# Kernel optimization log

Measured on AMD Instinct MI355X. Metric: run time of the kernel, lower is better.

The kernel has to match this reference:

```python
import jax, jax.numpy as jnp
import numpy as np

D_MODEL, D_STATE, D_CONV, EXPAND = 1024, 16, 4, 2
D_INNER = D_MODEL * EXPAND
BATCH, SEQ = 2, 1024
EPS = float(jnp.finfo(jnp.float32).eps)


def setup_inputs() -> dict:
    key = jax.random.key(0)
    ks = jax.random.split(key, 10)
    s = 0.02
    x = jax.random.normal(ks[0], (BATCH, SEQ, D_MODEL), jnp.float32)
    W_in = jax.random.normal(ks[1], (D_MODEL, 2 * D_INNER), jnp.float32) * s
    conv_w = jax.random.normal(ks[2], (D_INNER, 1, D_CONV), jnp.float32) * s  # depthwise OIH
    conv_b = jax.random.normal(ks[3], (D_INNER,), jnp.float32) * s
    W_xproj = jax.random.normal(ks[4], (D_INNER, 2 * D_STATE + 1), jnp.float32) * s
    W_dt = jax.random.normal(ks[5], (1, D_INNER), jnp.float32) * s
    b_dt = jax.random.normal(ks[6], (D_INNER,), jnp.float32) * s
    A_log = jnp.log(jnp.tile(jnp.arange(1, D_STATE + 1, dtype=jnp.float32), (D_INNER, 1)))
    D = jnp.ones((D_INNER,), jnp.float32)
    W_out = jax.random.normal(ks[7], (D_INNER, D_MODEL), jnp.float32) * s
    norm_w = jnp.ones((D_MODEL,), jnp.float32)
    return {"x": x, "W_in": W_in, "conv_w": conv_w, "conv_b": conv_b,
            "W_xproj": W_xproj, "W_dt": W_dt, "b_dt": b_dt,
            "A_log": A_log, "D": D, "W_out": W_out, "norm_w": norm_w}


def _rmsnorm(x, w):
    ms = jnp.mean(x * x, axis=-1, keepdims=True)
    return x * jax.lax.rsqrt(ms + EPS) * w


def _causal_depthwise_conv(x, w, b):
    # x: [B, d_inner, S], w: [d_inner, 1, d_conv] -> left-pad (d_conv-1), valid conv == torch pad+slice
    y = jax.lax.conv_general_dilated(
        x, w, window_strides=(1,), padding=[(D_CONV - 1, 0)],
        dimension_numbers=("NCH", "OIH", "NCH"), feature_group_count=D_INNER)
    return y + b[None, :, None]


def reference(x, W_in, conv_w, conv_b, W_xproj, W_dt, b_dt, A_log, D, W_out, norm_w):
    residual = x
    xn = _rmsnorm(x, norm_w)
    xz = xn @ W_in                                   # [B,S,2*d_inner]
    x_inner, z = jnp.split(xz, 2, axis=-1)
    xc = _causal_depthwise_conv(x_inner.transpose(0, 2, 1), conv_w, conv_b)
    x_conv = jax.nn.silu(xc.transpose(0, 2, 1))      # [B,S,d_inner]
    ssm = x_conv @ W_xproj                           # [B,S,2*d_state+1]
    dt_raw = ssm[..., :1]
    Bp = ssm[..., 1:1 + D_STATE]                     # [B,S,n]
    Cp = ssm[..., 1 + D_STATE:]                      # [B,S,n]
    dt = jax.nn.softplus(dt_raw @ W_dt + b_dt)       # [B,S,d_inner]
    A = -jnp.exp(A_log)                              # [d_inner,n]
    A_bar = jnp.exp(jnp.einsum("bsd,dn->bsdn", dt, A))
    B_bar = (dt * x_conv)[..., None] * Bp[:, :, None, :]  # [B,S,d,n]

    def step(h, inp):
        Ab, Bb, c = inp                              # [B,d,n],[B,d,n],[B,n]
        h = Ab * h + Bb
        y_t = jnp.einsum("bdn,bn->bd", h, c)
        return h, y_t

    h0 = jnp.zeros((x.shape[0], D_INNER, D_STATE), x.dtype)
    _, ys = jax.lax.scan(step, h0, (A_bar.transpose(1, 0, 2, 3),
                                    B_bar.transpose(1, 0, 2, 3),
                                    Cp.transpose(1, 0, 2)))
    y = ys.transpose(1, 0, 2) + x_conv * D           # [B,S,d_inner]
    y = y * jax.nn.silu(z)
    return residual + y @ W_out
```

## Files before the change

kernel.cpp:

```cpp
#include <hip/hip_runtime.h>
#include <hip/hip_bf16.h>
#include <cstddef>

__device__ __forceinline__ float bf2f(unsigned short u) {
    union { unsigned int i; float f; } c; c.i = ((unsigned int)u) << 16; return c.f;
}
__device__ __forceinline__ unsigned short f2bf(float f) {
    unsigned int u = __float_as_uint(f);
    u += 0x7fffu + ((u >> 16) & 1u);
    return (unsigned short)(u >> 16);
}

typedef __attribute__((ext_vector_type(8))) short short8;
typedef __attribute__((ext_vector_type(8))) unsigned short ushort8;
typedef __attribute__((ext_vector_type(4))) float floatx4;

__device__ __forceinline__ void gload_lds16(const void* gc, void* l) {
    void* g = const_cast<void*>(gc);
    __builtin_amdgcn_global_load_lds((__attribute__((address_space(1))) void*)g,
                                     (__attribute__((address_space(3))) void*)l,
                                     16, 0, 0);
}

#define B_      2
#define S_      1024
#define DM      1024
#define DI      2048
#define DS      16
#define NROW    (B_ * S_)
#define EPSF    1.1920928955078125e-07f
#define CCH     64
#define CLEN    (S_ / CCH)
#define NCHAIN  (B_ * DI * DS)
#define NDG     (B_ * DI / 256)
#define SCAN_GRID (NDG * CCH)

__device__ __forceinline__ void transpose_body(const float* __restrict__ in,
                                               unsigned short* __restrict__ out,
                                               int R, int C, int bx, int by,
                                               int tid, unsigned short (*tile)[33]) {
    int tx = tid & 31, ty = tid >> 5;
    #pragma unroll
    for (int i = 0; i < 32; i += 8) {
        int c = bx + tx;
        if (c < C) tile[ty + i][tx] = f2bf(in[(size_t)(by + ty + i) * C + c]);
    }
    __syncthreads();
    #pragma unroll
    for (int i = 0; i < 32; i += 8) {
        int oc = bx + ty + i;
        if (oc < C) out[(size_t)oc * R + by + tx] = tile[tx][ty + i];
    }
}

template<int TBM, int TBN, int TBK, bool RES>
__device__ __forceinline__ void gemm_body(unsigned short* As, unsigned short* Bs,
                                          const unsigned short* __restrict__ A,
                                          const unsigned short* __restrict__ Bt,
                                          void* __restrict__ Cv,
                                          const float* __restrict__ resid,
                                          int M, int N, int K, int bm, int bn, int tid) {
    constexpr int MI = TBM / 32;
    constexpr int NJ = TBN / 32;
    constexpr int PA = TBM * TBK / (8 * 256);
    constexpr int PB = TBN * TBK / (8 * 256);
    int wave = tid >> 6, lane = tid & 63;
    int wm = (wave >> 1) * (TBM / 2), wn = (wave & 1) * (TBN / 2);
    floatx4 acc[MI][NJ] = {};
    int fr = lane & 15, fk = (lane >> 4) * 8;
    for (int k0 = 0; k0 < K; k0 += TBK) {
        #pragma unroll
        for (int p = 0; p < PA; ++p) {
            int lin0 = p * 256 + wave * 64;
            int lin  = lin0 + lane;
            int pl   = lin / (TBM * 4);
            int rem  = lin - pl * (TBM * 4);
            int r = rem >> 2, kc = (rem & 3) * 8;
            gload_lds16(&A[(size_t)(bm + r) * K + k0 + pl * 32 + kc], &As[lin0 * 8]);
        }
        #pragma unroll
        for (int p = 0; p < PB; ++p) {
            int lin0 = p * 256 + wave * 64;
            int lin  = lin0 + lane;
            int pl   = lin / (TBN * 4);
            int rem  = lin - pl * (TBN * 4);
            int r = rem >> 2, kc = (rem & 3) * 8;
            gload_lds16(&Bt[(size_t)(bn + r) * K + k0 + pl * 32 + kc], &Bs[lin0 * 8]);
        }
        __syncthreads();
        #pragma unroll
        for (int pl = 0; pl < TBK / 32; pl++) {
            short8 af[MI], bfr[NJ];
            #pragma unroll
            for (int i = 0; i < MI; i++)
                af[i]  = *(const short8*)(&As[(pl * TBM + wm + i * 16 + fr) * 32 + fk]);
            #pragma unroll
            for (int j = 0; j < NJ; j++)
                bfr[j] = *(const short8*)(&Bs[(pl * TBN + wn + j * 16 + fr) * 32 + fk]);
            #pragma unroll
            for (int i = 0; i < MI; i++)
                #pragma unroll
                for (int j = 0; j < NJ; j++)
                    acc[i][j] = __builtin_amdgcn_mfma_f32_16x16x32_bf16(af[i], bfr[j], acc[i][j], 0, 0, 0);
        }
        __syncthreads();
    }
    int col = lane & 15, rq = (lane >> 4) * 4;
    #pragma unroll
    for (int i = 0; i < MI; i++) {
        #pragma unroll
        for (int j = 0; j < NJ; j++) {
            #pragma unroll
            for (int r = 0; r < 4; r++) {
                int row = bm + wm + i * 16 + rq + r;
                int cc  = bn + wn + j * 16 + col;
                float v = acc[i][j][r];
                size_t idx = (size_t)row * N + cc;
                if (RES) {
                    ((float*)Cv)[idx] = v + resid[idx];
                } else {
                    ((unsigned short*)Cv)[idx] = f2bf(v);
                }
            }
        }
    }
}

__global__ __launch_bounds__(256) void prep_k(const float* __restrict__ x,
                                              const float* __restrict__ norm_w,
                                              const float* __restrict__ W_in,
                                              unsigned short* __restrict__ xn,
                                              unsigned short* __restrict__ WinT) {
    int bid = blockIdx.x;
    int tid = threadIdx.x;
    if (bid < NROW) {
        __shared__ float wsum[4];
        __shared__ float scale_s;
        const float* xr = x + (size_t)bid * DM;
        float4 xv = *(const float4*)(xr + tid * 4);
        float ss = xv.x*xv.x + xv.y*xv.y + xv.z*xv.z + xv.w*xv.w;
        #pragma unroll
        for (int off = 1; off < 64; off <<= 1) ss += __shfl_xor(ss, off);
        int wave = tid >> 6, lane = tid & 63;
        if (lane == 0) wsum[wave] = ss;
        __syncthreads();
        if (tid == 0) {
            float t = wsum[0] + wsum[1] + wsum[2] + wsum[3];
            scale_s = rsqrtf(t / (float)DM + EPSF);
        }
        __syncthreads();
        float sc = scale_s;
        float4 wv = *(const float4*)(norm_w + tid * 4);
        ushort4 o;
        o.x = f2bf(xv.x * sc * wv.x);
        o.y = f2bf(xv.y * sc * wv.y);
        o.z = f2bf(xv.z * sc * wv.z);
        o.w = f2bf(xv.w * sc * wv.w);
        *(ushort4*)(xn + (size_t)bid * DM + tid * 4) = o;
        return;
    }
    __shared__ unsigned short tile[32][33];
    int r = bid - NROW;
    transpose_body(W_in, WinT, DM, 2 * DI, (r & 127) * 32, (r >> 7) * 32, tid, tile);
}

__global__ __launch_bounds__(256) void gemm1t_k(const unsigned short* __restrict__ xn,
                                                const unsigned short* __restrict__ WinT,
                                                unsigned short* __restrict__ xz,
                                                const float* __restrict__ W_out,
                                                const float* __restrict__ W_xp,
                                                unsigned short* __restrict__ WoutT,
                                                unsigned short* __restrict__ WxT) {
    __shared__ __align__(16) unsigned short pool[2 * 128 * 32 + 2 * 64 * 32];
    int bid = blockIdx.x, tid = threadIdx.x;
    if (bid >= 1024) {
        unsigned short (*tile)[33] = (unsigned short (*)[33])pool;
        int r0 = bid - 1024;
        if (r0 < 2048) {
            transpose_body(W_out, WoutT, DI, DM, (r0 & 31) * 32, (r0 >> 5) * 32, tid, tile);
        } else {
            int r = r0 - 2048;
            transpose_body(W_xp, WxT, DI, 33, (r & 1) * 32, (r >> 1) * 32, tid, tile);
        }
        return;
    }
    int bm = (bid >> 6) * 128, bn = (bid & 63) * 64;
    gemm_body<128, 64, 64, false>(pool, pool + 2 * 128 * 32,
                                  xn, WinT, xz, nullptr, NROW, 2 * DI, DM, bm, bn, tid);
}

template<int TBM, int TBN, int TBK, bool RES>
__global__ __launch_bounds__(256) void gemm_bt(const unsigned short* __restrict__ A,
                                               const unsigned short* __restrict__ Bt,
                                               void* __restrict__ Cv,
                                               const float* __restrict__ resid,
                                               int M, int N, int K) {
    __shared__ __align__(16) unsigned short As[(TBK / 32) * TBM * 32];
    __shared__ __align__(16) unsigned short Bs[(TBK / 32) * TBN * 32];
    gemm_body<TBM, TBN, TBK, RES>(As, Bs, A, Bt, Cv, resid, M, N, K,
                                  blockIdx.y * TBM, blockIdx.x * TBN, threadIdx.x);
}

__global__ __launch_bounds__(256) void convxproj_k(const unsigned short* __restrict__ xz,
                                                   const float* __restrict__ cw,
                                                   const float* __restrict__ cb,
                                                   const unsigned short* __restrict__ WxT,
                                                   unsigned short* __restrict__ xc,
                                                   float* __restrict__ ssm) {
    int row0 = blockIdx.x * 2;
    int s0   = row0 & (S_ - 1);
    int tid  = threadIdx.x;
    int d8   = tid * 8;
    int wave = tid >> 6, lane = tid & 63;
    float wt[8][4];
    #pragma unroll
    for (int j = 0; j < 8; j++) {
        float4 v = *(const float4*)(cw + (size_t)(d8 + j) * 4);
        wt[j][0] = v.x; wt[j][1] = v.y; wt[j][2] = v.z; wt[j][3] = v.w;
    }
    float4 cb0 = *(const float4*)(cb + d8);
    float4 cb1 = *(const float4*)(cb + d8 + 4);
    float bias[8] = { cb0.x, cb0.y, cb0.z, cb0.w, cb1.x, cb1.y, cb1.z, cb1.w };
    float xv[5][8];
    #pragma unroll
    for (int r = 0; r < 5; r++) {
        int s = s0 - 3 + r;
        if (s >= 0) {
            ushort8 u = *(const ushort8*)(xz + (size_t)(row0 - 3 + r) * (2 * DI) + d8);
            #pragma unroll
            for (int j = 0; j < 8; j++) xv[r][j] = bf2f(u[j]);
        } else {
            #pragma unroll
            for (int j = 0; j < 8; j++) xv[r][j] = 0.f;
        }
    }
    float a0[8], a1[8];
    ushort8 o0, o1;
    #pragma unroll
    for (int j = 0; j < 8; j++) {
        float c0 = bias[j], c1 = bias[j];
        #pragma unroll
        for (int k = 0; k < 4; k++) {
            c0 = fmaf(xv[k][j],     wt[j][k], c0);
            c1 = fmaf(xv[k + 1][j], wt[j][k], c1);
        }
        a0[j] = c0 / (1.f + __expf(-c0));
        a1[j] = c1 / (1.f + __expf(-c1));
        o0[j] = f2bf(a0[j]);
        o1[j] = f2bf(a1[j]);
    }
    *(ushort8*)(xc + (size_t)row0 * DI + d8)       = o0;
    *(ushort8*)(xc + (size_t)(row0 + 1) * DI + d8) = o1;
    float acc0[33], acc1[33];
    #pragma unroll
    for (int c = 0; c < 33; c++) {
        ushort8 w8 = *(const ushort8*)(WxT + (size_t)c * DI + d8);
        float s0v = 0.f, s1v = 0.f;
        #pragma unroll
        for (int j = 0; j < 8; j++) {
            float wv = bf2f(w8[j]);
            s0v = fmaf(a0[j], wv, s0v);
            s1v = fmaf(a1[j], wv, s1v);
        }
        acc0[c] = s0v; acc1[c] = s1v;
    }
    #pragma unroll
    for (int off = 1; off < 64; off <<= 1) {
        #pragma unroll
        for (int c = 0; c < 33; c++) {
            acc0[c] += __shfl_xor(acc0[c], off);
            acc1[c] += __shfl_xor(acc1[c], off);
        }
    }
    __shared__ float red0[4][33];
    __shared__ float red1[4][33];
    if (lane == 0) {
        #pragma unroll
        for (int c = 0; c < 33; c++) { red0[wave][c] = acc0[c]; red1[wave][c] = acc1[c]; }
    }
    __syncthreads();
    if (tid < 33) {
        ssm[(size_t)row0 * 33 + tid] =
            red0[0][tid] + red0[1][tid] + red0[2][tid] + red0[3][tid];
        ssm[(size_t)(row0 + 1) * 33 + tid] =
            red1[0][tid] + red1[1][tid] + red1[2][tid] + red1[3][tid];
    }
}

__device__ __forceinline__ float softplus_f(float x) {
    return fmaxf(x, 0.f) + __logf(1.f + __expf(-fabsf(x)));
}

__global__ __launch_bounds__(256) void scan_p1(const float* __restrict__ ssm,
                                               const unsigned short* __restrict__ xc,
                                               const float* __restrict__ Wdt,
                                               const float* __restrict__ bdt,
                                               unsigned short* __restrict__ Ph,
                                               unsigned short* __restrict__ hLh) {
    __shared__ float sbuf[CLEN * 33];
    int bid = blockIdx.x, tid = threadIdx.x;
    int c  = bid & (CCH - 1);
    int dg = bid >> 6;
    int b  = dg >> 3;
    int d  = ((dg & 7) << 8) + tid;
    int s0 = c * CLEN;
    const float* sp = ssm + ((size_t)b * S_ + s0) * 33;
    for (int i = tid; i < CLEN * 33; i += 256) sbuf[i] = sp[i];
    __syncthreads();
    float Wd = Wdt[d], bdv = bdt[d];
    const unsigned short* xp = xc + ((size_t)b * S_ + s0) * DI + d;
    float h[16];
    #pragma unroll
    for (int n = 0; n < 16; n++) h[n] = 0.f;
    float E = 1.f;
    for (int s = 0; s < CLEN; ++s) {
        float dtr = sbuf[s * 33];
        float xcv = bf2f(xp[(size_t)s * DI]);
        float dtv = softplus_f(fmaf(dtr, Wd, bdv));
        float e1  = __expf(-dtv);
        float dtx = dtv * xcv;
        E *= e1;
        float Ab = 1.f;
        #pragma unroll
        for (int n = 0; n < 16; n++) {
            Ab *= e1;
            h[n] = fmaf(Ab, h[n], dtx * sbuf[s * 33 + 1 + n]);
        }
    }
    size_t base = (size_t)c * NCHAIN + ((size_t)(b * DI + d) << 4);
    unsigned short Pv[16], hv[16];
    float Pn = 1.f;
    #pragma unroll
    for (int n = 0; n < 16; n++) { Pn *= E; Pv[n] = f2bf(Pn); hv[n] = f2bf(h[n]); }
    *(ushort8*)(&Ph[base])      = *(ushort8*)(&Pv[0]);
    *(ushort8*)(&Ph[base + 8])  = *(ushort8*)(&Pv[8]);
    *(ushort8*)(&hLh[base])     = *(ushort8*)(&hv[0]);
    *(ushort8*)(&hLh[base + 8]) = *(ushort8*)(&hv[8]);
}

__global__ __launch_bounds__(256) void scan_p2(const unsigned short* __restrict__ Ph,
                                               const unsigned short* __restrict__ hLh,
                                               unsigned short* __restrict__ hs) {
    int chain = blockIdx.x * 256 + threadIdx.x;
    float h = 0.f;
    #pragma unroll
    for (int c = 0; c < CCH; ++c) {
        size_t i = (size_t)c * NCHAIN + chain;
        hs[i] = f2bf(h);
        h = fmaf(bf2f(Ph[i]), h, bf2f(hLh[i]));
    }
}

__global__ __launch_bounds__(256) void scan_p3(const float* __restrict__ ssm,
                                               const unsigned short* __restrict__ xc,
                                               const unsigned short* __restrict__ xz,
                                               const float* __restrict__ Wdt,
                                               const float* __restrict__ bdt,
                                               const float* __restrict__ Dp,
                                               const unsigned short* __restrict__ hs,
                                               unsigned short* __restrict__ yg) {
    __shared__ float sbuf[CLEN * 33];
    int bid = blockIdx.x, tid = threadIdx.x;
    int c  = bid & (CCH - 1);
    int dg = bid >> 6;
    int b  = dg >> 3;
    int d  = ((dg & 7) << 8) + tid;
    int s0 = c * CLEN;
    const float* sp = ssm + ((size_t)b * S_ + s0) * 33;
    for (int i = tid; i < CLEN * 33; i += 256) sbuf[i] = sp[i];
    __syncthreads();
    float Wd = Wdt[d], bdv = bdt[d];
    float Dd = Dp[d];
    size_t base = (size_t)c * NCHAIN + ((size_t)(b * DI + d) << 4);
    ushort8 h0a = *(const ushort8*)(&hs[base]);
    ushort8 h0b = *(const ushort8*)(&hs[base + 8]);
    float h[16];
    #pragma unroll
    for (int n = 0; n < 8; n++) { h[n] = bf2f(h0a[n]); h[8 + n] = bf2f(h0b[n]); }
    const unsigned short* xp = xc + ((size_t)b * S_ + s0) * DI + d;
    const unsigned short* zp = xz + ((size_t)b * S_ + s0) * (2 * DI) + DI + d;
    unsigned short* yp = yg + ((size_t)b * S_ + s0) * DI + d;
    for (int s = 0; s < CLEN; ++s) {
        float dtr = sbuf[s * 33];
        float xcv = bf2f(xp[(size_t)s * DI]);
        float zv  = bf2f(zp[(size_t)s * (2 * DI)]);
        float dtv = softplus_f(fmaf(dtr, Wd, bdv));
        float e1  = __expf(-dtv);
        float dtx = dtv * xcv;
        float y   = xcv * Dd;
        float Ab  = 1.f;
        #pragma unroll
        for (int n = 0; n < 16; n++) {
            Ab *= e1;
            h[n] = fmaf(Ab, h[n], dtx * sbuf[s * 33 + 1 + n]);
            y    = fmaf(h[n], sbuf[s * 33 + 17 + n], y);
        }
        float gate = zv / (1.f + __expf(-zv));
        yp[(size_t)s * DI] = f2bf(y * gate);
    }
}

extern "C" void kernel_launch(void* const* d_in, const int* in_sizes, int n_in,
                              void* d_out, int out_size, void* d_ws, size_t ws_size,
                              hipStream_t stream) {
    const float* x      = (const float*)d_in[0];
    const float* W_in   = (const float*)d_in[1];
    const float* conv_w = (const float*)d_in[2];
    const float* conv_b = (const float*)d_in[3];
    const float* W_xp   = (const float*)d_in[4];
    const float* W_dt   = (const float*)d_in[5];
    const float* b_dt   = (const float*)d_in[6];
    const float* Dp     = (const float*)d_in[8];
    const float* W_out  = (const float*)d_in[9];
    const float* norm_w = (const float*)d_in[10];
    float* out = (float*)d_out;

    char* ws = (char*)d_ws;
    const size_t MB = 1024 * 1024;
    unsigned short* xn    = (unsigned short*)(ws + 0);
    unsigned short* WinT  = (unsigned short*)(ws + 4*MB);
    unsigned short* xz    = (unsigned short*)(ws + 12*MB);
    unsigned short* xc    = (unsigned short*)(ws + 28*MB);
    unsigned short* WoutT = (unsigned short*)(ws + 36*MB);
    unsigned short* yg    = (unsigned short*)(ws + 40*MB);
    float*          ssm   = (float*)        (ws + 48*MB);
    unsigned short* WxT   = (unsigned short*)(ws + 49*MB);
    unsigned short* Ph    = (unsigned short*)(ws + 50*MB);
    unsigned short* hLh   = (unsigned short*)(ws + 58*MB);
    unsigned short* hsh   = (unsigned short*)(ws + 66*MB);

    prep_k<<<NROW + 4096, 256, 0, stream>>>(x, norm_w, W_in, xn, WinT);
    gemm1t_k<<<1024 + 2048 + 128, 256, 0, stream>>>(xn, WinT, xz, W_out, W_xp, WoutT, WxT);
    convxproj_k<<<NROW / 2, 256, 0, stream>>>(xz, conv_w, conv_b, WxT, xc, ssm);
    scan_p1<<<SCAN_GRID, 256, 0, stream>>>(ssm, xc, W_dt, b_dt, Ph, hLh);
    scan_p2<<<NCHAIN / 256, 256, 0, stream>>>(Ph, hLh, hsh);
    scan_p3<<<SCAN_GRID, 256, 0, stream>>>(ssm, xc, xz, W_dt, b_dt, Dp, hsh, yg);
    gemm_bt<64, 64, 128, true><<<dim3(DM / 64, NROW / 64), 256, 0, stream>>>(
        yg, WoutT, out, x, NROW, DM, DI);
}
```

Baseline: 203.5 us.

## Fuse three-pass chunked scan into single decoupled-lookback kernel; widen in-proj GEMM tile

Replaces the three scan kernels (chunk summaries, serial carry propagation, re-scan with output) with one kernel. Each chunk block publishes its aggregate decay and state, then walks back through predecessor flags to build its inclusive prefix before emitting outputs. Flags are cleared in the conv/xproj kernel. Separately, the input-projection GEMM moves from 128x64 to 128x128 tiles to raise reuse. This removes two launches and the intermediate state round trip, but relies on forward progress of earlier blocks, adds spin-wait latency, and lowers GEMM block count.

```diff
diff --git a/kernel.cpp b/kernel.cpp
--- a/kernel.cpp
+++ b/kernel.cpp
@@ -32,8 +32,7 @@
 #define CCH     64
 #define CLEN    (S_ / CCH)
 #define NCHAIN  (B_ * DI * DS)
-#define NDG     (B_ * DI / 256)
-#define SCAN_GRID (NDG * CCH)
+#define SCAN_GRID 1024
 
 __device__ __forceinline__ void transpose_body(const float* __restrict__ in,
                                                unsigned short* __restrict__ out,
@@ -171,11 +170,11 @@
                                                 const float* __restrict__ W_xp,
                                                 unsigned short* __restrict__ WoutT,
                                                 unsigned short* __restrict__ WxT) {
-    __shared__ __align__(16) unsigned short pool[2 * 128 * 32 + 2 * 64 * 32];
+    __shared__ __align__(16) unsigned short pool[2 * 128 * 32 * 2];
     int bid = blockIdx.x, tid = threadIdx.x;
-    if (bid >= 1024) {
+    if (bid >= 512) {
         unsigned short (*tile)[33] = (unsigned short (*)[33])pool;
-        int r0 = bid - 1024;
+        int r0 = bid - 512;
         if (r0 < 2048) {
             transpose_body(W_out, WoutT, DI, DM, (r0 & 31) * 32, (r0 >> 5) * 32, tid, tile);
         } else {
@@ -184,9 +183,9 @@
         }
         return;
     }
-    int bm = (bid >> 6) * 128, bn = (bid & 63) * 64;
-    gemm_body<128, 64, 64, false>(pool, pool + 2 * 128 * 32,
-                                  xn, WinT, xz, nullptr, NROW, 2 * DI, DM, bm, bn, tid);
+    int bm = (bid >> 5) * 128, bn = (bid & 31) * 128;
+    gemm_body<128, 128, 64, false>(pool, pool + 2 * 128 * 32,
+                                   xn, WinT, xz, nullptr, NROW, 2 * DI, DM, bm, bn, tid);
 }
 
 template<int TBM, int TBN, int TBK, bool RES>
@@ -206,7 +205,9 @@
                                                    const float* __restrict__ cb,
                                                    const unsigned short* __restrict__ WxT,
                                                    unsigned short* __restrict__ xc,
-                                                   float* __restrict__ ssm) {
+                                                   float* __restrict__ ssm,
+                                                   unsigned int* __restrict__ flags) {
+    if (threadIdx.x == 0) flags[blockIdx.x] = 0u;
     int row0 = blockIdx.x * 2;
     int s0   = row0 & (S_ - 1);
     int tid  = threadIdx.x;
@@ -291,24 +292,31 @@
     return fmaxf(x, 0.f) + __logf(1.f + __expf(-fabsf(x)));
 }
 
-__global__ __launch_bounds__(256) void scan_p1(const float* __restrict__ ssm,
-                                               const unsigned short* __restrict__ xc,
-                                               const float* __restrict__ Wdt,
-                                               const float* __restrict__ bdt,
-                                               unsigned short* __restrict__ Ph,
-                                               unsigned short* __restrict__ hLh) {
+__global__ __launch_bounds__(256, 4) void scan_one(const float* __restrict__ ssm,
+                                                   const unsigned short* __restrict__ xc,
+                                                   const unsigned short* __restrict__ xz,
+                                                   const float* __restrict__ Wdt,
+                                                   const float* __restrict__ bdt,
+                                                   const float* __restrict__ Dp,
+                                                   unsigned short* __restrict__ aggP,
+                                                   unsigned short* __restrict__ aggH,
+                                                   unsigned short* __restrict__ incH,
+                                                   unsigned int* __restrict__ flags,
+                                                   unsigned short* __restrict__ yg) {
     __shared__ float sbuf[CLEN * 33];
+    __shared__ unsigned int sflag;
     int bid = blockIdx.x, tid = threadIdx.x;
     int c  = bid & (CCH - 1);
     int dg = bid >> 6;
     int b  = dg >> 3;
     int d  = ((dg & 7) << 8) + tid;
-    int s0 = c * CLEN;
-    const float* sp = ssm + ((size_t)b * S_ + s0) * 33;
+    int s0c = c * CLEN;
+    const float* sp = ssm + ((size_t)b * S_ + s0c) * 33;
     for (int i = tid; i < CLEN * 33; i += 256) sbuf[i] = sp[i];
     __syncthreads();
     float Wd = Wdt[d], bdv = bdt[d];
-    const unsigned short* xp = xc + ((size_t)b * S_ + s0) * DI + d;
+    float Dd = Dp[d];
+    const unsigned short* xp = xc + ((size_t)b * S_ + s0c) * DI + d;
     float h[16];
     #pragma unroll
     for (int n = 0; n < 16; n++) h[n] = 0.f;
@@ -327,59 +335,89 @@
             h[n] = fmaf(Ab, h[n], dtx * sbuf[s * 33 + 1 + n]);
         }
     }
-    size_t base = (size_t)c * NCHAIN + ((size_t)(b * DI + d) << 4);
-    unsigned short Pv[16], hv[16];
-    float Pn = 1.f;
-    #pragma unroll
-    for (int n = 0; n < 16; n++) { Pn *= E; Pv[n] = f2bf(Pn); hv[n] = f2bf(h[n]); }
-    *(ushort8*)(&Ph[base])      = *(ushort8*)(&Pv[0]);
-    *(ushort8*)(&Ph[base + 8])  = *(ushort8*)(&Pv[8]);
-    *(ushort8*)(&hLh[base])     = *(ushort8*)(&hv[0]);
-    *(ushort8*)(&hLh[base + 8]) = *(ushort8*)(&hv[8]);
-}
-
-__global__ __launch_bounds__(256) void scan_p2(const unsigned short* __restrict__ Ph,
-                                               const unsigned short* __restrict__ hLh,
-                                               unsigned short* __restrict__ hs) {
-    int chain = blockIdx.x * 256 + threadIdx.x;
-    float h = 0.f;
-    #pragma unroll
-    for (int c = 0; c < CCH; ++c) {
-        size_t i = (size_t)c * NCHAIN + chain;
-        hs[i] = f2bf(h);
-        h = fmaf(bf2f(Ph[i]), h, bf2f(hLh[i]));
-    }
-}
-
-__global__ __launch_bounds__(256) void scan_p3(const float* __restrict__ ssm,
-                                               const unsigned short* __restrict__ xc,
-                                               const unsigned short* __restrict__ xz,
-                                               const float* __restrict__ Wdt,
-                                               const float* __restrict__ bdt,
-                                               const float* __restrict__ Dp,
-                                               const unsigned short* __restrict__ hs,
-                                               unsigned short* __restrict__ yg) {
-    __shared__ float sbuf[CLEN * 33];
-    int bid = blockIdx.x, tid = threadIdx.x;
-    int c  = bid & (CCH - 1);
-    int dg = bid >> 6;
-    int b  = dg >> 3;
-    int d  = ((dg & 7) << 8) + tid;
-    int s0 = c * CLEN;
-    const float* sp = ssm + ((size_t)b * S_ + s0) * 33;
-    for (int i = tid; i < CLEN * 33; i += 256) sbuf[i] = sp[i];
+    float P[16];
+    {
+        float Pn = 1.f;
+        #pragma unroll
+        for (int n = 0; n < 16; n++) { Pn *= E; P[n] = Pn; }
+    }
+    size_t base = (size_t)bid * 4096 + tid * 16;
+    {
+        unsigned short Pv[16], hv[16];
+        #pragma unroll
+        for (int n = 0; n < 16; n++) { Pv[n] = f2bf(P[n]); hv[n] = f2bf(h[n]); }
+        *(ushort8*)(&aggP[base])     = *(ushort8*)(&Pv[0]);
+        *(ushort8*)(&aggP[base + 8]) = *(ushort8*)(&Pv[8]);
+        *(ushort8*)(&aggH[base])     = *(ushort8*)(&hv[0]);
+        *(ushort8*)(&aggH[base + 8]) = *(ushort8*)(&hv[8]);
+    }
+    __threadfence();
     __syncthreads();
-    float Wd = Wdt[d], bdv = bdt[d];
-    float Dd = Dp[d];
-    size_t base = (size_t)c * NCHAIN + ((size_t)(b * DI + d) << 4);
-    ushort8 h0a = *(const ushort8*)(&hs[base]);
-    ushort8 h0b = *(const ushort8*)(&hs[base + 8]);
-    float h[16];
-    #pragma unroll
-    for (int n = 0; n < 8; n++) { h[n] = bf2f(h0a[n]); h[8 + n] = bf2f(h0b[n]); }
-    const unsigned short* xp = xc + ((size_t)b * S_ + s0) * DI + d;
-    const unsigned short* zp = xz + ((size_t)b * S_ + s0) * (2 * DI) + DI + d;
-    unsigned short* yp = yg + ((size_t)b * S_ + s0) * DI + d;
+    if (tid == 0)
+        __hip_atomic_store(&flags[bid], (c == 0) ? 2u : 1u,
+                           __ATOMIC_RELEASE, __HIP_MEMORY_SCOPE_AGENT);
+    float h0[16], coef[16];
+    #pragma unroll
+    for (int n = 0; n < 16; n++) { h0[n] = 0.f; coef[n] = 1.f; }
+    if (c > 0) {
+        for (int j = c - 1; j >= 0; --j) {
+            if (tid == 0) {
+                unsigned int f;
+                do {
+                    f = __hip_atomic_load(&flags[(dg << 6) + j],
+                                          __ATOMIC_ACQUIRE, __HIP_MEMORY_SCOPE_AGENT);
+                    if (f == 0) __builtin_amdgcn_s_sleep(1);
+                } while (f == 0);
+                sflag = f;
+            }
+            __syncthreads();
+            unsigned int f = sflag;
+            __syncthreads();
+            size_t jb = ((size_t)((dg << 6) + j)) * 4096 + tid * 16;
+            if (f == 2u) {
+                ushort8 ia = *(const ushort8*)(&incH[jb]);
+                ushort8 ib = *(const ushort8*)(&incH[jb + 8]);
+                #pragma unroll
+                for (int n = 0; n < 8; n++) {
+                    h0[n]     = fmaf(coef[n],     bf2f(ia[n]), h0[n]);
+                    h0[8 + n] = fmaf(coef[8 + n], bf2f(ib[n]), h0[8 + n]);
+                }
+                break;
+            } else {
+                ushort8 pa = *(const ushort8*)(&aggP[jb]);
+                ushort8 pb = *(const ushort8*)(&aggP[jb + 8]);
+                ushort8 ha = *(const ushort8*)(&aggH[jb]);
+                ushort8 hb = *(const ushort8*)(&aggH[jb + 8]);
+                #pragma unroll
+                for (int n = 0; n < 8; n++) {
+                    h0[n]     = fmaf(coef[n],     bf2f(ha[n]), h0[n]);
+                    h0[8 + n] = fmaf(coef[8 + n], bf2f(hb[n]), h0[8 + n]);
+                    coef[n]     *= bf2f(pa[n]);
+                    coef[8 + n] *= bf2f(pb[n]);
+                }
+            }
+        }
+        unsigned short iv[16];
+        #pragma unroll
+        for (int n = 0; n < 16; n++) iv[n] = f2bf(fmaf(P[n], h0[n], h[n]));
+        *(ushort8*)(&incH[base])     = *(ushort8*)(&iv[0]);
+        *(ushort8*)(&incH[base + 8]) = *(ushort8*)(&iv[8]);
+        __threadfence();
+        __syncthreads();
+        if (tid == 0)
+            __hip_atomic_store(&flags[bid], 2u,
+                               __ATOMIC_RELEASE, __HIP_MEMORY_SCOPE_AGENT);
+    } else {
+        unsigned short iv[16];
+        #pragma unroll
+        for (int n = 0; n < 16; n++) iv[n] = f2bf(h[n]);
+        *(ushort8*)(&incH[base])     = *(ushort8*)(&iv[0]);
+        *(ushort8*)(&incH[base + 8]) = *(ushort8*)(&iv[8]);
+    }
+    #pragma unroll
+    for (int n = 0; n < 16; n++) h[n] = bf2f(f2bf(h0[n]));
+    const unsigned short* zp = xz + ((size_t)b * S_ + s0c) * (2 * DI) + DI + d;
+    unsigned short* yp = yg + ((size_t)b * S_ + s0c) * DI + d;
     for (int s = 0; s < CLEN; ++s) {
         float dtr = sbuf[s * 33];
         float xcv = bf2f(xp[(size_t)s * DI]);
@@ -425,16 +463,16 @@
     unsigned short* yg    = (unsigned short*)(ws + 40*MB);
     float*          ssm   = (float*)        (ws + 48*MB);
     unsigned short* WxT   = (unsigned short*)(ws + 49*MB);
-    unsigned short* Ph    = (unsigned short*)(ws + 50*MB);
-    unsigned short* hLh   = (unsigned short*)(ws + 58*MB);
-    unsigned short* hsh   = (unsigned short*)(ws + 66*MB);
+    unsigned short* aggP  = (unsigned short*)(ws + 50*MB);
+    unsigned short* aggH  = (unsigned short*)(ws + 58*MB);
+    unsigned short* incH  = (unsigned short*)(ws + 66*MB);
+    unsigned int*   flags = (unsigned int*)  (ws + 74*MB);
 
     prep_k<<<NROW + 4096, 256, 0, stream>>>(x, norm_w, W_in, xn, WinT);
-    gemm1t_k<<<1024 + 2048 + 128, 256, 0, stream>>>(xn, WinT, xz, W_out, W_xp, WoutT, WxT);
-    convxproj_k<<<NROW / 2, 256, 0, stream>>>(xz, conv_w, conv_b, WxT, xc, ssm);
-    scan_p1<<<SCAN_GRID, 256, 0, stream>>>(ssm, xc, W_dt, b_dt, Ph, hLh);
-    scan_p2<<<NCHAIN / 256, 256, 0, stream>>>(Ph, hLh, hsh);
-    scan_p3<<<SCAN_GRID, 256, 0, stream>>>(ssm, xc, xz, W_dt, b_dt, Dp, hsh, yg);
+    gemm1t_k<<<512 + 2048 + 128, 256, 0, stream>>>(xn, WinT, xz, W_out, W_xp, WoutT, WxT);
+    convxproj_k<<<NROW / 2, 256, 0, stream>>>(xz, conv_w, conv_b, WxT, xc, ssm, flags);
+    scan_one<<<SCAN_GRID, 256, 0, stream>>>(ssm, xc, xz, W_dt, b_dt, Dp,
+                                            aggP, aggH, incH, flags, yg);
     gemm_bt<64, 64, 128, true><<<dim3(DM / 64, NROW / 64), 256, 0, stream>>>(
         yg, WoutT, out, x, NROW, DM, DI);
 }
```

Measured after the change: 613.7 us. +201.6%, slower.
